# Kernel optimization log

Hardware: AMD Instinct MI355X
Metric: run time of the kernel (lower is better)

The kernel has to match this reference:

```python
import jax, jax.numpy as jnp
import numpy as np

N_NODES = 100000
N_EDGES = 1600000
N_FEATS = 9
HIDDEN = 64
DIM_OUT = 1
N_GRAPHS = 512
EPS_MSG = 1e-7   # GENConv message eps
BN_EPS = 1e-5    # BatchNorm1d eps


def _lin(key, fan_in, fan_out):
    kw, kb = jax.random.split(key)
    s = 1.0 / np.sqrt(fan_in)
    w = jax.random.uniform(kw, (fan_in, fan_out), jnp.float32, -s, s)
    b = jax.random.uniform(kb, (fan_out,), jnp.float32, -s, s)
    return w, b


def setup_inputs() -> dict:
    key = jax.random.key(0)
    ks = jax.random.split(key, 32)
    inp = {}
    inp["x"] = jax.random.normal(ks[0], (N_NODES, N_FEATS), jnp.float32)
    inp["edge_index"] = jax.random.randint(ks[1], (2, N_EDGES), 0, N_NODES, jnp.int64)
    inp["batch_idx"] = jnp.sort(jax.random.randint(ks[2], (N_NODES,), 0, N_GRAPHS, jnp.int64))
    # conv1 input projections (in != out)
    inp["w_src"], inp["b_src"] = _lin(ks[3], N_FEATS, HIDDEN)
    inp["w_dst"], inp["b_dst"] = _lin(ks[4], N_FEATS, HIDDEN)
    # per-conv MLP: Linear(H,2H) -> BN(2H) -> ReLU -> Linear(2H,H)
    for i, k in zip((1, 2, 3), (ks[5], ks[6], ks[7])):
        k1, k2 = jax.random.split(k)
        w1, b1 = _lin(k1, HIDDEN, 2 * HIDDEN)
        w2, b2 = _lin(k2, 2 * HIDDEN, HIDDEN)
        inp[f"w1_{i}"], inp[f"b1_{i}"] = w1, b1
        inp[f"g_{i}"] = jnp.ones((2 * HIDDEN,), jnp.float32)
        inp[f"be_{i}"] = jnp.zeros((2 * HIDDEN,), jnp.float32)
        inp[f"w2_{i}"], inp[f"b2_{i}"] = w2, b2
    inp["w_dense"], inp["b_dense"] = _lin(ks[8], HIDDEN, DIM_OUT)
    return inp


def _seg_softmax(m, idx, n):
    # per-channel softmax over edges sharing the same destination node
    mx = jax.ops.segment_max(m, idx, num_segments=n)
    e = jnp.exp(m - mx[idx])
    s = jax.ops.segment_sum(e, idx, num_segments=n)
    return e / (s[idx] + 1e-16)


def _mlp(h, w1, b1, g, be, w2, b2):
    h = h @ w1 + b1                                   # [N, 2H]
    mu = jnp.mean(h, axis=0)
    var = jnp.var(h, axis=0)
    h = (h - mu) * jax.lax.rsqrt(var + BN_EPS) * g + be
    return jax.nn.relu(h) @ w2 + b2                   # [N, H]


def _genconv(x_src, x_dst, src, dst, w1, b1, g, be, w2, b2):
    n = x_dst.shape[0]
    msg = jax.nn.relu(x_src[src]) + EPS_MSG           # [E, H] gather + message
    alpha = _seg_softmax(msg, dst, n)                 # softmax aggregation, t=1
    aggr = jax.ops.segment_sum(alpha * msg, dst, num_segments=n)
    return _mlp(aggr + x_dst, w1, b1, g, be, w2, b2)


def reference(x, edge_index, batch_idx, w_src, b_src, w_dst, b_dst,
              w1_1, b1_1, g_1, be_1, w2_1, b2_1,
              w1_2, b1_2, g_2, be_2, w2_2, b2_2,
              w1_3, b1_3, g_3, be_3, w2_3, b2_3,
              w_dense, b_dense):
    src, dst = edge_index[0], edge_index[1]
    h = jax.nn.relu(_genconv(x @ w_src + b_src, x @ w_dst + b_dst, src, dst,
                             w1_1, b1_1, g_1, be_1, w2_1, b2_1))
    h = jax.nn.relu(_genconv(h, h, src, dst, w1_2, b1_2, g_2, be_2, w2_2, b2_2))
    h = jax.nn.relu(_genconv(h, h, src, dst, w1_3, b1_3, g_3, be_3, w2_3, b2_3))
    # global mean pool over graphs
    tot = jax.ops.segment_sum(h, batch_idx, num_segments=N_GRAPHS)
    cnt = jax.ops.segment_sum(jnp.ones((h.shape[0],), h.dtype), batch_idx, num_segments=N_GRAPHS)
    pooled = tot / jnp.maximum(cnt, 1.0)[:, None]     # [G, H]
    return jax.nn.sigmoid(pooled @ w_dense + b_dense) # [G, 1]
```

## Files before the change

### kernel.cpp

```cpp
#include <hip/hip_runtime.h>

typedef unsigned short ushort_t;
typedef __attribute__((ext_vector_type(8))) short bf16x8;
typedef __attribute__((ext_vector_type(4))) float f32x4;

__device__ __forceinline__ unsigned short f2bf(float f){
  unsigned u = __float_as_uint(f);
  u = (u + 0x7FFFu + ((u >> 16) & 1u)) >> 16;
  return (unsigned short)u;
}
__device__ __forceinline__ float bf2f(unsigned short h){
  return __uint_as_float(((unsigned)h) << 16);
}


__global__ __launch_bounds__(256) void k_bhist(const int* __restrict__ dst, int* __restrict__ bcnt,
                                               int E, int NB){
  __shared__ int l[512];
  int t = threadIdx.x;
  for(int b=t; b<NB; b+=256) l[b] = 0;
  __syncthreads();
  int base = blockIdx.x*4096;
  #pragma unroll
  for(int r=0;r<16;++r){
    int i = base + r*256 + t;
    if(i < E){
      int d = __builtin_nontemporal_load(dst + i);
      atomicAdd(&l[d >> 8], 1);
    }
  }
  __syncthreads();
  for(int b=t; b<NB; b+=256){
    int c = l[b];
    if(c) atomicAdd(&bcnt[b], c);
  }
}

__global__ __launch_bounds__(512) void k_bscan(const int* __restrict__ bcnt, int* __restrict__ bbase,
                                               int* __restrict__ bcur, int* __restrict__ rp,
                                               int NB, int N, int E){
  __shared__ int s[512];
  int t = threadIdx.x;
  int v = (t < NB) ? bcnt[t] : 0;
  s[t] = v;
  __syncthreads();
  for(int off=1; off<512; off<<=1){
    int x = 0;
    if(t >= off) x = s[t-off];
    __syncthreads();
    if(t >= off) s[t] += x;
    __syncthreads();
  }
  int excl = s[t] - v;
  if(t < NB){ bbase[t] = excl; bcur[t] = excl; }
  if(t == NB-1) bbase[NB] = excl + v;
  if(t == 0) rp[N] = E;
}

__global__ __launch_bounds__(256) void k_part(const int* __restrict__ src, const int* __restrict__ dst,
                                              int* __restrict__ bcur, unsigned* __restrict__ ebuf,
                                              int E, int NB){
  __shared__ int lcnt[512];
  __shared__ int lbase[512];
  int t = threadIdx.x;
  int base = blockIdx.x * 4096;
  for(int b=t; b<NB; b+=256) lcnt[b] = 0;
  __syncthreads();

  int srcv[16], dstv[16];
  #pragma unroll
  for(int r=0;r<16;++r){
    int i = base + r*256 + t;
    if(i < E){
      srcv[r] = __builtin_nontemporal_load(src + i);
      dstv[r] = __builtin_nontemporal_load(dst + i);
    } else dstv[r] = -1;
  }
  #pragma unroll
  for(int r=0;r<16;++r)
    if(dstv[r] >= 0) atomicAdd(&lcnt[dstv[r] >> 8], 1);
  __syncthreads();
  for(int b=t; b<NB; b+=256){
    int c = lcnt[b];
    lbase[b] = c ? atomicAdd(&bcur[b], c) : 0;
    lcnt[b] = 0;
  }
  __syncthreads();
  #pragma unroll
  for(int r=0;r<16;++r){
    if(dstv[r] >= 0){
      int b = dstv[r] >> 8;
      int p = lbase[b] + atomicAdd(&lcnt[b], 1);
      ebuf[p] = (((unsigned)dstv[r] & 255u) << 17) | (unsigned)srcv[r];
    }
  }
}

__global__ __launch_bounds__(256) void k_place(const int* __restrict__ bbase, const unsigned* __restrict__ ebuf,
                                               int* __restrict__ esrc, int* __restrict__ rp, int N){
  __shared__ int lcnt[256];
  __shared__ int sc[256];
  __shared__ int lcur[256];
  int t = threadIdx.x;
  int b = blockIdx.x;
  int n0 = b << 8;
  int e0 = bbase[b], e1 = bbase[b+1];
  lcnt[t] = 0;
  __syncthreads();
  for(int i = e0 + t; i < e1; i += 256)
    atomicAdd(&lcnt[ebuf[i] >> 17], 1);
  __syncthreads();
  int v = lcnt[t];
  sc[t] = v;
  __syncthreads();
  for(int off=1; off<256; off<<=1){
    int x = 0;
    if(t >= off) x = sc[t-off];
    __syncthreads();
    if(t >= off) sc[t] += x;
    __syncthreads();
  }
  int rpv = e0 + sc[t] - v;
  if(n0 + t < N) rp[n0 + t] = rpv;
  lcur[t] = rpv;
  __syncthreads();
  for(int i = e0 + t; i < e1; i += 256){
    unsigned w = ebuf[i];
    int dl = (int)(w >> 17);
    int p = atomicAdd(&lcur[dl], 1);
    esrc[p] = (int)(w & 0x1FFFFu);
  }
}

__global__ __launch_bounds__(256) void k_wconv(const float* __restrict__ w1a, const float* __restrict__ w2a,
                                               const float* __restrict__ w1b, const float* __restrict__ w2b,
                                               const float* __restrict__ w1c, const float* __restrict__ w2c,
                                               ushort_t* __restrict__ w1t, ushort_t* __restrict__ w2t){
  int L = blockIdx.x >> 6;
  const float* w1 = (L==0) ? w1a : (L==1) ? w1b : w1c;
  const float* w2 = (L==0) ? w2a : (L==1) ? w2b : w2c;
  int t = (blockIdx.x & 63)*256 + threadIdx.x;
  if(t < 8192){
    int n = t >> 6, k = t & 63;
    w1t[L*8192 + n*64 + k] = f2bf(w1[k*128 + n]);
  } else {
    int i = t - 8192;
    int n = i >> 7, k = i & 127;
    w2t[L*8192 + n*128 + k] = f2bf(w2[k*64 + n]);
  }
}

__global__ __launch_bounds__(256) void k_proj(const float* __restrict__ x,
                                              const float* __restrict__ ws, const float* __restrict__ bs,
                                              const float* __restrict__ wd, const float* __restrict__ bd,
                                              ushort_t* __restrict__ hd16, ushort_t* __restrict__ gs16, int N){
  int gid = blockIdx.x*256 + threadIdx.x;
  int n = gid >> 6, c = gid & 63;
  if(n >= N) return;
  float as = bs[c], ad = bd[c];
  const float* xr = x + (size_t)n*9;
  #pragma unroll
  for(int k=0;k<9;++k){
    float xv = xr[k];
    as += xv * ws[k*64 + c];
    ad += xv * wd[k*64 + c];
  }
  hd16[(size_t)n*64 + c] = f2bf(ad);
  gs16[(size_t)n*64 + c] = f2bf(fmaxf(as, 0.f));
}

__global__ __launch_bounds__(256) void k_emlp1(const ushort_t* __restrict__ gs, const ushort_t* __restrict__ xd16,
                                               const int* __restrict__ rp, const int* __restrict__ es,
                                               const ushort_t* __restrict__ w1t, const float* __restrict__ b1,
                                               ushort_t* __restrict__ h1, float* __restrict__ part, int N){
  __shared__ ushort_t yt[32*72];
  __shared__ ushort_t cs[32*136];
  __shared__ float lds_s[128];
  __shared__ float lds_q[128];
  int t = threadIdx.x;
  int w = t >> 6, lane = t & 63;
  int nbase = blockIdx.x * 32;

  const ushort_t* gl = gs + lane;
  for(int i=0;i<8;++i){
    int nl = w*8 + i;
    int n = nbase + nl;
    float aggr = 0.f;
    if(n < N){
      int beg = __builtin_amdgcn_readfirstlane(rp[n]);
      int end = __builtin_amdgcn_readfirstlane(rp[n+1]);
      float S[8], T[8];
      #pragma unroll
      for(int j=0;j<8;++j){ S[j]=0.f; T[j]=0.f; }
      int nfull = beg + ((end - beg) & ~7);
      int base = beg;
      for(; base < nfull; base += 8){
        float g[8];
        #pragma unroll
        for(int j=0;j<8;++j){
          int idx = __builtin_amdgcn_readfirstlane(es[base+j]);
          g[j] = bf2f(gl[(size_t)idx*64]) + 1e-7f;
        }
        #pragma unroll
        for(int j=0;j<8;++j){
          float p = __expf(g[j]);
          S[j] += p; T[j] += p*g[j];
        }
      }
      if(base < end){
        float g[8];
        #pragma unroll
        for(int j=0;j<8;++j){
          int e = base + j;
          int idx = __builtin_amdgcn_readfirstlane(es[e < end ? e : end-1]);
          g[j] = bf2f(gl[(size_t)idx*64]) + 1e-7f;
        }
        #pragma unroll
        for(int j=0;j<8;++j){
          float p = (base + j < end) ? __expf(g[j]) : 0.f;
          S[j] += p; T[j] += p*g[j];
        }
      }
      float Ss = ((S[0]+S[1])+(S[2]+S[3])) + ((S[4]+S[5])+(S[6]+S[7]));
      float Ts = ((T[0]+T[1])+(T[2]+T[3])) + ((T[4]+T[5])+(T[6]+T[7]));
      aggr = Ts/(Ss + 1e-16f) + bf2f(xd16[(size_t)n*64 + lane]);
    }
    yt[nl*72 + lane] = f2bf(aggr);
  }
  __syncthreads();

  int ln = lane & 15, quad = lane >> 4;
  bf16x8 B[2][2];
  #pragma unroll
  for(int c=0;c<2;++c){
    int n = (2*w+c)*16 + ln;
    #pragma unroll
    for(int q=0;q<2;++q)
      B[c][q] = *(const bf16x8*)(w1t + n*64 + q*32 + quad*8);
  }

  f32x4 z = {0.f,0.f,0.f,0.f};
  f32x4 acc[2][2] = {{z,z},{z,z}};
  #pragma unroll
  for(int q=0;q<2;++q){
    #pragma unroll
    for(int tt=0;tt<2;++tt){
      bf16x8 A = *(const bf16x8*)(yt + (tt*16 + ln)*72 + q*32 + quad*8);
      #pragma unroll
      for(int c=0;c<2;++c)
        acc[tt][c] = __builtin_amdgcn_mfma_f32_16x16x32_bf16(A, B[c][q], acc[tt][c], 0,0,0);
    }
  }

  float s[2] = {0.f, 0.f}, qq[2] = {0.f, 0.f};
  #pragma unroll
  for(int c=0;c<2;++c){
    int n = (2*w+c)*16 + ln;
    float bb = b1[n];
    #pragma unroll
    for(int tt=0;tt<2;++tt){
      #pragma unroll
      for(int r=0;r<4;++r){
        int row = tt*16 + quad*4 + r;
        float v = acc[tt][c][r] + bb;
        bool ok = (nbase + row) < N;
        s[c]  += ok ? v   : 0.f;
        qq[c] += ok ? v*v : 0.f;
        cs[row*136 + n] = f2bf(v);
      }
    }
  }
  #pragma unroll
  for(int c=0;c<2;++c){
    float vs = s[c], vq = qq[c];
    vs += __shfl_down(vs, 32, 64); vs += __shfl_down(vs, 16, 64);
    vq += __shfl_down(vq, 32, 64); vq += __shfl_down(vq, 16, 64);
    if(quad == 0){
      lds_s[(2*w+c)*16 + ln] = vs;
      lds_q[(2*w+c)*16 + ln] = vq;
    }
  }
  __syncthreads();
  #pragma unroll
  for(int r2=0;r2<2;++r2){
    int idx = r2*256 + t;
    int row = idx >> 4, c8 = (idx & 15)*8;
    int m = nbase + row;
    if(m < N)
      *(uint4*)(h1 + (size_t)m*128 + c8) = *(const uint4*)(cs + row*136 + c8);
  }
  if(t < 128) part[(size_t)blockIdx.x*256 + t] = lds_s[t];
  else        part[(size_t)blockIdx.x*256 + t] = lds_q[t-128];
}

__global__ __launch_bounds__(256) void k_bnred2(const float* __restrict__ part, float* __restrict__ bnp, int nblk){
  int t = threadIdx.x;
  float a = 0.f;
  for(int b = blockIdx.x; b < nblk; b += 32) a += part[(size_t)b*256 + t];
  bnp[blockIdx.x*256 + t] = a;
}

__global__ __launch_bounds__(128) void k_bnfold(const float* __restrict__ bnp, const float* __restrict__ g,
                                                const float* __restrict__ be, float* __restrict__ sb, float invN){
  int j = threadIdx.x;
  float s = 0.f, q = 0.f;
  for(int b=0;b<32;++b){ s += bnp[b*256 + j]; q += bnp[b*256 + 128 + j]; }
  float mu = s*invN;
  float var = q*invN - mu*mu;
  float sc = g[j] * rsqrtf(var + 1e-5f);
  sb[j] = sc;
  sb[128+j] = be[j] - mu*sc;
}

__global__ __launch_bounds__(256) void k_mlp2(const ushort_t* __restrict__ h1, const float* __restrict__ sb,
                                              const ushort_t* __restrict__ w2t, const float* __restrict__ b2,
                                              ushort_t* __restrict__ h16, int N){
  __shared__ ushort_t act[64*136];
  __shared__ ushort_t cs2[64*72];
  int t = threadIdx.x;
  int n0 = blockIdx.x*64;
  #pragma unroll
  for(int r=0;r<4;++r){
    int idx = r*256 + t;
    int row = idx >> 4, k8 = (idx & 15)*8;
    int n = n0 + row;
    ushort_t tmp[8];
    if(n < N){
      *(uint4*)tmp = *(const uint4*)(h1 + (size_t)n*128 + k8);
    } else {
      #pragma unroll
      for(int j=0;j<8;++j) tmp[j] = 0;
    }
    #pragma unroll
    for(int j=0;j<8;++j){
      float v = bf2f(tmp[j]) * sb[k8+j] + sb[128+k8+j];
      tmp[j] = f2bf(fmaxf(v, 0.f));
    }
    *(uint4*)(act + row*136 + k8) = *(uint4*)tmp;
  }
  __syncthreads();
  int w = t >> 6, lane = t & 63;
  int ln = lane & 15, quad = lane >> 4;

  int n = w*16 + ln;
  bf16x8 B[4];
  #pragma unroll
  for(int q=0;q<4;++q)
    B[q] = *(const bf16x8*)(w2t + n*128 + q*32 + quad*8);

  f32x4 z = {0.f,0.f,0.f,0.f};
  f32x4 acc[4] = {z,z,z,z};
  #pragma unroll
  for(int q=0;q<4;++q){
    #pragma unroll
    for(int tt=0;tt<4;++tt){
      bf16x8 A = *(const bf16x8*)(act + (tt*16 + ln)*136 + q*32 + quad*8);
      acc[tt] = __builtin_amdgcn_mfma_f32_16x16x32_bf16(A, B[q], acc[tt], 0,0,0);
    }
  }
  float bb = b2[n];
  #pragma unroll
  for(int tt=0;tt<4;++tt){
    #pragma unroll
    for(int r=0;r<4;++r){
      int row = tt*16 + quad*4 + r;
      float v = fmaxf(acc[tt][r] + bb, 0.f);
      cs2[row*72 + n] = f2bf(v);
    }
  }
  __syncthreads();
  #pragma unroll
  for(int r2=0;r2<2;++r2){
    int idx = r2*256 + t;
    int row = idx >> 3, c8 = (idx & 7)*8;
    int m = n0 + row;
    if(m < N)
      *(uint4*)(h16 + (size_t)m*64 + c8) = *(const uint4*)(cs2 + row*72 + c8);
  }
}

__device__ __forceinline__ int lbound(const int* a, int n, int key){
  int lo = 0, hi = n;
  while(lo < hi){
    int mid = (lo + hi) >> 1;
    if(a[mid] < key) lo = mid + 1; else hi = mid;
  }
  return lo;
}

__global__ __launch_bounds__(256) void k_pool(const ushort_t* __restrict__ h16, const int* __restrict__ batch,
                                              const float* __restrict__ wd, const float* __restrict__ bd,
                                              float* __restrict__ out, int N){
  int g = blockIdx.x;
  int lo = lbound(batch, N, g);
  int hi = lbound(batch, N, g+1);
  int c = threadIdx.x & 63, w = threadIdx.x >> 6;
  float acc = 0.f;
  for(int n = lo + w; n < hi; n += 4) acc += bf2f(h16[(size_t)n*64 + c]);
  __shared__ float red[4][64];
  red[w][c] = acc;
  __syncthreads();
  if(w == 0){
    float v = red[0][c] + red[1][c] + red[2][c] + red[3][c];
    float count = (float)(hi - lo);
    v = v / fmaxf(count, 1.f) * wd[c];
    for(int off=32; off>0; off>>=1) v += __shfl_down(v, off, 64);
    if(c == 0) out[g] = 1.f / (1.f + expf(-(v + bd[0])));
  }
}


extern "C" void kernel_launch(void* const* d_in, const int* in_sizes, int n_in,
                              void* d_out, int out_size, void* d_ws, size_t ws_size,
                              hipStream_t stream){
  const float* x      = (const float*)d_in[0];
  const int*   ei     = (const int*)  d_in[1];
  const int*   batch  = (const int*)  d_in[2];
  const float* w_src  = (const float*)d_in[3];
  const float* b_src  = (const float*)d_in[4];
  const float* w_dst  = (const float*)d_in[5];
  const float* b_dst  = (const float*)d_in[6];
  const float* w_dense= (const float*)d_in[25];
  const float* b_dense= (const float*)d_in[26];
  float* out = (float*)d_out;

  const int N = in_sizes[2];
  const int E = in_sizes[1] / 2;
  const int* src = ei;
  const int* dst = ei + E;

  char* ws = (char*)d_ws;
  size_t off = 0;
  auto take = [&](size_t bytes) -> void* {
    void* p = ws + off;
    off += (bytes + 255) & ~(size_t)255;
    return p;
  };
  const int nblk1 = (N + 31) / 32;
  ushort_t* hd16 = (ushort_t*)take((size_t)N*64*2);
  ushort_t* gs16 = (ushort_t*)take((size_t)N*64*2);
  ushort_t* h1   = (ushort_t*)take((size_t)N*128*2);
  ushort_t* h16  = (ushort_t*)take((size_t)N*64*2);
  unsigned* ebuf = (unsigned*)take((size_t)E*4);
  int*      esrc = (int*)     take((size_t)E*4);
  int*      rp   = (int*)     take((size_t)(N+1)*4);
  int*      bcnt = (int*)     take(512*4);
  int*      bbase= (int*)     take(520*4);
  int*      bcur = (int*)     take(512*4);
  float*    bnp  = (float*)   take(32*256*4);
  float*    sb   = (float*)   take(256*4);
  float*    part = (float*)   take((size_t)nblk1*256*4);
  ushort_t* w1t  = (ushort_t*)take(3*8192*2);
  ushort_t* w2t  = (ushort_t*)take(3*8192*2);

  const int gN64  = (N*64 + 255) / 256;
  const int NB    = (N + 255) >> 8;
  const int nchnk = (E + 4095) / 4096;

  k_wconv<<<192, 256, 0, stream>>>(
    (const float*)d_in[7],  (const float*)d_in[11],
    (const float*)d_in[13], (const float*)d_in[17],
    (const float*)d_in[19], (const float*)d_in[23],
    w1t, w2t);

  (void)hipMemsetAsync(bcnt, 0, 512*4, stream);
  k_bhist<<<nchnk, 256, 0, stream>>>(dst, bcnt, E, NB);
  k_bscan<<<1,     512, 0, stream>>>(bcnt, bbase, bcur, rp, NB, N, E);
  k_part <<<nchnk, 256, 0, stream>>>(src, dst, bcur, ebuf, E, NB);
  k_place<<<NB,    256, 0, stream>>>(bbase, ebuf, esrc, rp, N);

  k_proj<<<gN64, 256, 0, stream>>>(x, w_src, b_src, w_dst, b_dst, hd16, gs16, N);

  const ushort_t* gs_l[3] = { gs16, h16, h16 };
  const ushort_t* xd_l[3] = { hd16, h16, h16 };
  const float invN = 1.0f / (float)N;

  for(int L=0; L<3; ++L){
    const float* b1 = (const float*)d_in[7 + 6*L + 1];
    const float* g  = (const float*)d_in[7 + 6*L + 2];
    const float* be = (const float*)d_in[7 + 6*L + 3];
    const float* b2 = (const float*)d_in[7 + 6*L + 5];

    k_emlp1<<<nblk1, 256, 0, stream>>>(gs_l[L], xd_l[L], rp, esrc, w1t + L*8192, b1, h1, part, N);
    k_bnred2<<<32, 256, 0, stream>>>(part, bnp, nblk1);
    k_bnfold<<<1,  128, 0, stream>>>(bnp, g, be, sb, invN);
    k_mlp2<<<(N+63)/64, 256, 0, stream>>>(h1, sb, w2t + L*8192, b2, h16, N);
  }

  k_pool<<<512, 256, 0, stream>>>(h16, batch, w_dense, b_dense, out, N);
}
```

Before: 513.8 us.

## Fuse BN partial reduction into emlp1 via atomics and vectorize edge loads

The BatchNorm statistics reduction kernel is removed. Each emlp1 block now atomically adds its per-column sums and sums of squares into one of 32 slices. bnfold zeroes the slices after use, and the initial memset is extended to cover them. Separately, the histogram and partition kernels now load 16 contiguous edges per thread with 128-bit nontemporal loads instead of strided scalar loads. The gains are one fewer launch per layer and wider edge reads, paid for with atomic contention on the slices and float summation order that is no longer deterministic.

After: 429.4 us. -16.4%, faster.

```diff
diff --git a/kernel.cpp b/kernel.cpp
--- a/kernel.cpp
+++ b/kernel.cpp
@@ -3,6 +3,7 @@
 typedef unsigned short ushort_t;
 typedef __attribute__((ext_vector_type(8))) short bf16x8;
 typedef __attribute__((ext_vector_type(4))) float f32x4;
+typedef __attribute__((ext_vector_type(4))) int int4v;
 
 __device__ __forceinline__ unsigned short f2bf(float f){
   unsigned u = __float_as_uint(f);
@@ -20,14 +21,16 @@
   int t = threadIdx.x;
   for(int b=t; b<NB; b+=256) l[b] = 0;
   __syncthreads();
-  int base = blockIdx.x*4096;
-  #pragma unroll
-  for(int r=0;r<16;++r){
-    int i = base + r*256 + t;
-    if(i < E){
-      int d = __builtin_nontemporal_load(dst + i);
-      atomicAdd(&l[d >> 8], 1);
-    }
+  int base = blockIdx.x*4096 + t*16;
+  if(base + 16 <= E){
+    #pragma unroll
+    for(int r=0;r<4;++r){
+      int4v d = __builtin_nontemporal_load((const int4v*)(dst + base + r*4));
+      atomicAdd(&l[d.x >> 8], 1); atomicAdd(&l[d.y >> 8], 1);
+      atomicAdd(&l[d.z >> 8], 1); atomicAdd(&l[d.w >> 8], 1);
+    }
+  } else {
+    for(int i=base; i<E; ++i) atomicAdd(&l[dst[i] >> 8], 1);
   }
   __syncthreads();
   for(int b=t; b<NB; b+=256){
@@ -63,18 +66,24 @@
   __shared__ int lcnt[512];
   __shared__ int lbase[512];
   int t = threadIdx.x;
-  int base = blockIdx.x * 4096;
+  int base = blockIdx.x*4096 + t*16;
   for(int b=t; b<NB; b+=256) lcnt[b] = 0;
   __syncthreads();
 
   int srcv[16], dstv[16];
-  #pragma unroll
-  for(int r=0;r<16;++r){
-    int i = base + r*256 + t;
-    if(i < E){
-      srcv[r] = __builtin_nontemporal_load(src + i);
-      dstv[r] = __builtin_nontemporal_load(dst + i);
-    } else dstv[r] = -1;
+  if(base + 16 <= E){
+    #pragma unroll
+    for(int r=0;r<4;++r){
+      *(int4v*)(dstv + r*4) = __builtin_nontemporal_load((const int4v*)(dst + base + r*4));
+      *(int4v*)(srcv + r*4) = __builtin_nontemporal_load((const int4v*)(src + base + r*4));
+    }
+  } else {
+    #pragma unroll
+    for(int k=0;k<16;++k){
+      int i = base + k;
+      if(i < E){ dstv[k] = dst[i]; srcv[k] = src[i]; }
+      else dstv[k] = -1;
+    }
   }
   #pragma unroll
   for(int r=0;r<16;++r)
@@ -172,11 +181,9 @@
 __global__ __launch_bounds__(256) void k_emlp1(const ushort_t* __restrict__ gs, const ushort_t* __restrict__ xd16,
                                                const int* __restrict__ rp, const int* __restrict__ es,
                                                const ushort_t* __restrict__ w1t, const float* __restrict__ b1,
-                                               ushort_t* __restrict__ h1, float* __restrict__ part, int N){
+                                               ushort_t* __restrict__ h1, float* __restrict__ bnp, int N){
   __shared__ ushort_t yt[32*72];
   __shared__ ushort_t cs[32*136];
-  __shared__ float lds_s[128];
-  __shared__ float lds_q[128];
   int t = threadIdx.x;
   int w = t >> 6, lane = t & 63;
   int nbase = blockIdx.x * 32;
@@ -270,14 +277,18 @@
       }
     }
   }
-  #pragma unroll
-  for(int c=0;c<2;++c){
-    float vs = s[c], vq = qq[c];
-    vs += __shfl_down(vs, 32, 64); vs += __shfl_down(vs, 16, 64);
-    vq += __shfl_down(vq, 32, 64); vq += __shfl_down(vq, 16, 64);
-    if(quad == 0){
-      lds_s[(2*w+c)*16 + ln] = vs;
-      lds_q[(2*w+c)*16 + ln] = vq;
+  {
+    float* slice = bnp + (size_t)(blockIdx.x & 31)*256;
+    #pragma unroll
+    for(int c=0;c<2;++c){
+      float vs = s[c], vq = qq[c];
+      vs += __shfl_down(vs, 32, 64); vs += __shfl_down(vs, 16, 64);
+      vq += __shfl_down(vq, 32, 64); vq += __shfl_down(vq, 16, 64);
+      if(quad == 0){
+        int col = (2*w+c)*16 + ln;
+        atomicAdd(&slice[col], vs);
+        atomicAdd(&slice[128+col], vq);
+      }
     }
   }
   __syncthreads();
@@ -289,18 +300,9 @@
     if(m < N)
       *(uint4*)(h1 + (size_t)m*128 + c8) = *(const uint4*)(cs + row*136 + c8);
   }
-  if(t < 128) part[(size_t)blockIdx.x*256 + t] = lds_s[t];
-  else        part[(size_t)blockIdx.x*256 + t] = lds_q[t-128];
-}
-
-__global__ __launch_bounds__(256) void k_bnred2(const float* __restrict__ part, float* __restrict__ bnp, int nblk){
-  int t = threadIdx.x;
-  float a = 0.f;
-  for(int b = blockIdx.x; b < nblk; b += 32) a += part[(size_t)b*256 + t];
-  bnp[blockIdx.x*256 + t] = a;
-}
-
-__global__ __launch_bounds__(128) void k_bnfold(const float* __restrict__ bnp, const float* __restrict__ g,
+}
+
+__global__ __launch_bounds__(128) void k_bnfold(float* __restrict__ bnp, const float* __restrict__ g,
                                                 const float* __restrict__ be, float* __restrict__ sb, float invN){
   int j = threadIdx.x;
   float s = 0.f, q = 0.f;
@@ -310,6 +312,7 @@
   float sc = g[j] * rsqrtf(var + 1e-5f);
   sb[j] = sc;
   sb[128+j] = be[j] - mu*sc;
+  for(int b=0;b<32;++b){ bnp[b*256 + j] = 0.f; bnp[b*256 + 128 + j] = 0.f; }
 }
 
 __global__ __launch_bounds__(256) void k_mlp2(const ushort_t* __restrict__ h1, const float* __restrict__ sb,
@@ -436,7 +439,6 @@
     off += (bytes + 255) & ~(size_t)255;
     return p;
   };
-  const int nblk1 = (N + 31) / 32;
   ushort_t* hd16 = (ushort_t*)take((size_t)N*64*2);
   ushort_t* gs16 = (ushort_t*)take((size_t)N*64*2);
   ushort_t* h1   = (ushort_t*)take((size_t)N*128*2);
@@ -445,14 +447,14 @@
   int*      esrc = (int*)     take((size_t)E*4);
   int*      rp   = (int*)     take((size_t)(N+1)*4);
   int*      bcnt = (int*)     take(512*4);
+  float*    bnp  = (float*)   take(32*256*4);
   int*      bbase= (int*)     take(520*4);
   int*      bcur = (int*)     take(512*4);
-  float*    bnp  = (float*)   take(32*256*4);
   float*    sb   = (float*)   take(256*4);
-  float*    part = (float*)   take((size_t)nblk1*256*4);
   ushort_t* w1t  = (ushort_t*)take(3*8192*2);
   ushort_t* w2t  = (ushort_t*)take(3*8192*2);
 
+  const int nblk1 = (N + 31) / 32;
   const int gN64  = (N*64 + 255) / 256;
   const int NB    = (N + 255) >> 8;
   const int nchnk = (E + 4095) / 4096;
@@ -463,7 +465,8 @@
     (const float*)d_in[19], (const float*)d_in[23],
     w1t, w2t);
 
-  (void)hipMemsetAsync(bcnt, 0, 512*4, stream);
+  (void)hipMemsetAsync(bcnt, 0, 512*4 + 32*256*4, stream);
+
   k_bhist<<<nchnk, 256, 0, stream>>>(dst, bcnt, E, NB);
   k_bscan<<<1,     512, 0, stream>>>(bcnt, bbase, bcur, rp, NB, N, E);
   k_part <<<nchnk, 256, 0, stream>>>(src, dst, bcur, ebuf, E, NB);
@@ -481,9 +484,8 @@
     const float* be = (const float*)d_in[7 + 6*L + 3];
     const float* b2 = (const float*)d_in[7 + 6*L + 5];
 
-    k_emlp1<<<nblk1, 256, 0, stream>>>(gs_l[L], xd_l[L], rp, esrc, w1t + L*8192, b1, h1, part, N);
-    k_bnred2<<<32, 256, 0, stream>>>(part, bnp, nblk1);
-    k_bnfold<<<1,  128, 0, stream>>>(bnp, g, be, sb, invN);
+    k_emlp1<<<nblk1, 256, 0, stream>>>(gs_l[L], xd_l[L], rp, esrc, w1t + L*8192, b1, h1, bnp, N);
+    k_bnfold<<<1, 128, 0, stream>>>(bnp, g, be, sb, invN);
     k_mlp2<<<(N+63)/64, 256, 0, stream>>>(h1, sb, w2t + L*8192, b2, h16, N);
   }
 
```
